# Kernel optimization log

Measured on AMD Instinct MI355X. Metric: run time of the kernel, lower is better.

Reference implementation:

```python
import jax, jax.numpy as jnp
import numpy as np

HIDDEN = 2048
NUM_HEADS = 16
NUM_KV_HEADS = 8
HEAD_DIM = 128
Q_SIZE = NUM_HEADS * HEAD_DIM          # 2048
KV_SIZE = NUM_KV_HEADS * HEAD_DIM      # 1024
ROPE_THETA = 1000000.0
RMS_EPS = 1e-6
SCALE = HEAD_DIM ** -0.5


def setup_inputs() -> dict:
    key = jax.random.key(0)
    k1, k2, k3 = jax.random.split(key, 3)
    T = 4096
    positions = jnp.arange(T, dtype=jnp.int64) if jax.config.jax_enable_x64 else jnp.arange(T, dtype=jnp.int32)
    hidden_states = jax.random.normal(k1, (T, HIDDEN), dtype=jnp.float32)
    qkv_w = jax.random.normal(k2, (Q_SIZE + 2 * KV_SIZE, HIDDEN), dtype=jnp.float32) * 0.02
    o_w = jax.random.normal(k3, (HIDDEN, Q_SIZE), dtype=jnp.float32) * 0.02
    q_norm_w = jnp.ones((HEAD_DIM,), dtype=jnp.float32)
    k_norm_w = jnp.ones((HEAD_DIM,), dtype=jnp.float32)
    return {
        "hidden_states": hidden_states,
        "qkv_w": qkv_w,
        "q_norm_w": q_norm_w,
        "k_norm_w": k_norm_w,
        "o_w": o_w,
        "positions": positions,
    }


def _rms_norm(x, w, eps=RMS_EPS):
    # per-head RMSNorm over last dim (head_dim)
    var = jnp.mean(jnp.square(x), axis=-1, keepdims=True)
    return x * jax.lax.rsqrt(var + eps) * w


def _rope(x, positions):
    # neox-style (rotate-half) RoPE. x: [T, H, D], positions: [T]
    D = x.shape[-1]
    inv_freq = 1.0 / (ROPE_THETA ** (jnp.arange(0, D, 2, dtype=jnp.float32) / D))  # [D/2]
    freqs = positions.astype(jnp.float32)[:, None] * inv_freq                      # [T, D/2]
    cos = jnp.cos(freqs)[:, None, :]  # [T, 1, D/2]
    sin = jnp.sin(freqs)[:, None, :]
    x1, x2 = x[..., : D // 2], x[..., D // 2 :]
    return jnp.concatenate([x1 * cos - x2 * sin, x2 * cos + x1 * sin], axis=-1)


def reference(hidden_states, qkv_w, q_norm_w, k_norm_w, o_w, positions):
    T = hidden_states.shape[0]
    qkv = hidden_states @ qkv_w.T                                   # [T, Q+2KV]
    q = qkv[:, :Q_SIZE].reshape(T, NUM_HEADS, HEAD_DIM)
    k = qkv[:, Q_SIZE : Q_SIZE + KV_SIZE].reshape(T, NUM_KV_HEADS, HEAD_DIM)
    v = qkv[:, Q_SIZE + KV_SIZE :].reshape(T, NUM_KV_HEADS, HEAD_DIM)

    # attention_bias=False path: per-head QK RMSNorm
    q = _rms_norm(q, q_norm_w)
    k = _rms_norm(k, k_norm_w)

    q = _rope(q, positions)
    k = _rope(k, positions)

    # GQA: expand KV heads to query heads
    rep = NUM_HEADS // NUM_KV_HEADS
    k = jnp.repeat(k, rep, axis=1)   # [T, H, D]
    v = jnp.repeat(v, rep, axis=1)

    scores = jnp.einsum("qhd,khd->hqk", q, k) * SCALE               # [H, T, T]
    causal = positions[:, None] >= positions[None, :]               # [T, T]
    scores = jnp.where(causal[None], scores, jnp.finfo(scores.dtype).min)
    probs = jax.nn.softmax(scores, axis=-1)
    attn = jnp.einsum("hqk,khd->qhd", probs, v)                     # [T, H, D]
    return attn.reshape(T, Q_SIZE) @ o_w.T                          # [T, HIDDEN]
```

## Files before the change

### kernel.cpp

```cpp
#include <hip/hip_runtime.h>
#include <hip/hip_bf16.h>
#include <math.h>


typedef __bf16 bf16;
typedef __bf16 bf16x4 __attribute__((ext_vector_type(4)));
typedef __bf16 bf16x8 __attribute__((ext_vector_type(8)));
typedef float  f32x4  __attribute__((ext_vector_type(4)));

__device__ __forceinline__ f32x4 mfma16(bf16x8 a, bf16x8 b, f32x4 c) {
  return __builtin_amdgcn_mfma_f32_16x16x32_bf16(a, b, c, 0, 0, 0);
}

__device__ __forceinline__ void mfma16x16_chain4(const bf16x4& a0, const bf16x4& a1,
                                                 const bf16x4& a2, const bf16x4& a3,
                                                 const bf16x4& b0, const bf16x4& b1,
                                                 const bf16x4& b2, const bf16x4& b3,
                                                 f32x4& c) {
  asm volatile(
      "s_nop 2\n\t"
      "v_mfma_f32_16x16x16_bf16 %0, %1, %5, %0\n\t"
      "v_mfma_f32_16x16x16_bf16 %0, %2, %6, %0\n\t"
      "v_mfma_f32_16x16x16_bf16 %0, %3, %7, %0\n\t"
      "v_mfma_f32_16x16x16_bf16 %0, %4, %8, %0"
      : "+v"(c)
      : "v"(a0), "v"(a1), "v"(a2), "v"(a3),
        "v"(b0), "v"(b1), "v"(b2), "v"(b3));
}

__device__ __forceinline__ void gload_lds16(const bf16* g, bf16* l) {
  __builtin_amdgcn_global_load_lds(
      (const __attribute__((address_space(1))) unsigned int*)g,
      (__attribute__((address_space(3))) unsigned int*)l, 16, 0, 0);
}

__device__ __forceinline__ void store_c(float* p, float v) { *p = v; }
__device__ __forceinline__ void store_c(bf16* p, float v) { *p = (bf16)v; }

__global__ __launch_bounds__(256) void cast_bf16(const float* __restrict__ s,
                                                 bf16* __restrict__ d) {
  int i = blockIdx.x * 256 + threadIdx.x;
  float4 a = reinterpret_cast<const float4*>(s)[i * 2];
  float4 b = reinterpret_cast<const float4*>(s)[i * 2 + 1];
  bf16x8 v = {(bf16)a.x, (bf16)a.y, (bf16)a.z, (bf16)a.w,
              (bf16)b.x, (bf16)b.y, (bf16)b.z, (bf16)b.w};
  reinterpret_cast<bf16x8*>(d)[i] = v;
}

__device__ __forceinline__ void gemm_step(const bf16* AsL, const bf16* BsL,
                                          int wm, int wn, int l16, int quad,
                                          f32x4 (&acc)[4][4]) {
  bf16x8 af[4], bfr[4];
#pragma unroll
  for (int i = 0; i < 4; ++i)
    af[i] = *reinterpret_cast<const bf16x8*>(&AsL[(wm + i * 16 + l16) * 32 + quad * 8]);
#pragma unroll
  for (int j = 0; j < 4; ++j)
    bfr[j] = *reinterpret_cast<const bf16x8*>(&BsL[(wn + j * 16 + l16) * 32 + quad * 8]);
#pragma unroll
  for (int i = 0; i < 4; ++i)
#pragma unroll
    for (int j = 0; j < 4; ++j)
      acc[i][j] = mfma16(af[i], bfr[j], acc[i][j]);
}

template <typename TC>
__global__ __launch_bounds__(256, 4) void gemm_bt(const bf16* __restrict__ A,
                                                  const bf16* __restrict__ B,
                                                  TC* __restrict__ C,
                                                  int M, int N, int K) {
  __shared__ __align__(16) bf16 As[2][128 * 32];
  __shared__ __align__(16) bf16 Bs[2][128 * 32];

  const int tid  = threadIdx.x;
  const int wave = tid >> 6, lane = tid & 63;
  const int quad = lane >> 4, l16 = lane & 15;
  const int wm = (wave >> 1) * 64, wn = (wave & 1) * 64;
  const int n0 = blockIdx.x * 128, m0 = blockIdx.y * 128;

  const int r0 = tid >> 2;
  const int c0 = (tid & 3) * 8;
  const size_t aBase = (size_t)(m0 + r0) * K + c0;
  const size_t bBase = (size_t)(n0 + r0) * K + c0;
  const size_t rowK64 = (size_t)64 * K;

  const f32x4 zero = {0.f, 0.f, 0.f, 0.f};
  f32x4 acc[4][4];
#pragma unroll
  for (int i = 0; i < 4; ++i)
#pragma unroll
    for (int j = 0; j < 4; ++j) acc[i][j] = zero;

  gload_lds16(&A[aBase],          &As[0][tid * 8]);
  gload_lds16(&A[aBase + rowK64], &As[0][2048 + tid * 8]);
  gload_lds16(&B[bBase],          &Bs[0][tid * 8]);
  gload_lds16(&B[bBase + rowK64], &Bs[0][2048 + tid * 8]);
  __syncthreads();

  int cur = 0;
  for (int k0 = 32; k0 < K; k0 += 32) {
    const int nb = cur ^ 1;
    gload_lds16(&A[aBase + k0],          &As[nb][tid * 8]);
    gload_lds16(&A[aBase + rowK64 + k0], &As[nb][2048 + tid * 8]);
    gload_lds16(&B[bBase + k0],          &Bs[nb][tid * 8]);
    gload_lds16(&B[bBase + rowK64 + k0], &Bs[nb][2048 + tid * 8]);

    gemm_step(As[cur], Bs[cur], wm, wn, l16, quad, acc);

    __syncthreads();
    cur = nb;
  }
  gemm_step(As[cur], Bs[cur], wm, wn, l16, quad, acc);

#pragma unroll
  for (int i = 0; i < 4; ++i)
#pragma unroll
    for (int j = 0; j < 4; ++j)
#pragma unroll
      for (int r = 0; r < 4; ++r) {
        int row = m0 + wm + i * 16 + quad * 4 + r;
        int col = n0 + wn + j * 16 + l16;
        store_c(&C[(size_t)row * N + col], acc[i][j][r]);
      }
}

__global__ __launch_bounds__(256) void norm_rope(const bf16* __restrict__ qkv,
                                                 const float* __restrict__ qw,
                                                 const float* __restrict__ kw,
                                                 const int* __restrict__ pos,
                                                 bf16* __restrict__ qn,
                                                 bf16* __restrict__ kn) {
  const int t = blockIdx.x;
  const int wv = threadIdx.x >> 6, l = threadIdx.x & 63;

  float inv = exp2f((float)l * (-19.93156856932417f / 64.0f));
  float fr = (float)pos[t] * inv;
  float sn, cs;
  sincosf(fr, &sn, &cs);
  const float qw1 = qw[l], qw2 = qw[l + 64];
  const float kw1 = kw[l], kw2 = kw[l + 64];
  const size_t rowb = (size_t)t * 4096;

#pragma unroll
  for (int i = 0; i < 6; ++i) {
    const int h = wv * 6 + i;
    const bool isq = h < 16;
    const int col = isq ? h * 128 : 2048 + (h - 16) * 128;
    float x1 = (float)qkv[rowb + col + l];
    float x2 = (float)qkv[rowb + col + l + 64];
    float ss = x1 * x1 + x2 * x2;
#pragma unroll
    for (int o = 32; o >= 1; o >>= 1) ss += __shfl_xor(ss, o);
    float rms = rsqrtf(ss * (1.0f / 128.0f) + 1e-6f);
    float w1 = isq ? qw1 : kw1, w2 = isq ? qw2 : kw2;
    float xn1 = x1 * rms * w1, xn2 = x2 * rms * w2;
    float o1 = xn1 * cs - xn2 * sn;
    float o2 = xn2 * cs + xn1 * sn;
    if (isq) {
      qn[(size_t)t * 2048 + h * 128 + l] = (bf16)o1;
      qn[(size_t)t * 2048 + h * 128 + l + 64] = (bf16)o2;
    } else {
      kn[(size_t)t * 1024 + (h - 16) * 128 + l] = (bf16)o1;
      kn[(size_t)t * 1024 + (h - 16) * 128 + l + 64] = (bf16)o2;
    }
  }
}

__global__ __launch_bounds__(256) void transpose_v(const bf16* __restrict__ qkv,
                                                   bf16* __restrict__ vt) {
  __shared__ __align__(16) bf16 tile[128 * 72];
  const int t0 = blockIdx.x * 64, kvh = blockIdx.y;
  const int tid = threadIdx.x;
#pragma unroll
  for (int it = 0; it < 2; ++it) {
    int linear = it * 4096 + tid * 16;
    int r = linear >> 7, c = linear & 127;
    union { uint4 v; bf16 e[8]; } u0, u1;
    u0.v = *reinterpret_cast<const uint4*>(
        &qkv[(size_t)(t0 + r) * 4096 + 3072 + kvh * 128 + c]);
    u1.v = *reinterpret_cast<const uint4*>(
        &qkv[(size_t)(t0 + r) * 4096 + 3072 + kvh * 128 + c + 8]);
#pragma unroll
    for (int j = 0; j < 8; ++j) tile[(c + j) * 72 + r] = u0.e[j];
#pragma unroll
    for (int j = 0; j < 8; ++j) tile[(c + 8 + j) * 72 + r] = u1.e[j];
  }
  __syncthreads();
#pragma unroll
  for (int it = 0; it < 4; ++it) {
    int linear = it * 2048 + tid * 8;
    int d = linear >> 6, c = linear & 63;
    uint4 v = *reinterpret_cast<const uint4*>(&tile[d * 72 + c]);
    *reinterpret_cast<uint4*>(&vt[(size_t)(kvh * 128 + d) * 4096 + t0 + c]) = v;
  }
}

__global__ __launch_bounds__(256, 2) void attn(const bf16* __restrict__ q,
                                               const bf16* __restrict__ k,
                                               const bf16* __restrict__ vt,
                                               bf16* __restrict__ out) {
  __shared__ __align__(16) bf16 Ks[2][64 * 128];
  __shared__ __align__(16) bf16 Vs[2][128 * 64];

  const int head = blockIdx.y, kvh = head >> 1;
  const int bx = blockIdx.x;

  const int tid = threadIdx.x;
  const int wave = tid >> 6, lane = tid & 63;
  const int quad = lane >> 4, l16 = lane & 15;
  const float cExp = 0.08838834764831845f * 1.4426950408889634f;
  const f32x4 zero = {0.f, 0.f, 0.f, 0.f};

  int kSrc[4], vSrc[4];
#pragma unroll
  for (int it = 0; it < 4; ++it) {
    int r = (wave * 4 + it) * 4 + (lane >> 4);
    kSrc[it] = r * 1024 + kvh * 128 + (((lane & 15) ^ (r & 7)) << 3);
    int d = (wave * 4 + it) * 8 + (lane >> 3);
    vSrc[it] = (kvh * 128 + d) * 4096 + (((lane & 7) ^ (lane >> 3)) << 3);
  }

  const int kswz = (l16 & 7) << 3;
  int koff[4], voff[4];
#pragma unroll
  for (int s = 0; s < 4; ++s) {
    koff[s] = (s * 32 + quad * 8) ^ kswz;
    voff[s] = (s * 16 + quad * 4) ^ kswz;
  }

#pragma unroll
  for (int it = 0; it < 4; ++it) {
    gload_lds16(&k[kSrc[it]], &Ks[0][(wave * 4 + it) * 512]);
    gload_lds16(&vt[vSrc[it]], &Vs[0][(wave * 4 + it) * 512]);
  }
  int cur = 0;

#pragma unroll
  for (int phase = 0; phase < 2; ++phase) {
    const int qt = phase == 0 ? bx : 63 - bx;
    const int q0 = qt * 64;
    const int kend = q0 + 64;
    const int qrow = q0 + wave * 16 + l16;

    bf16x8 qf[4];
#pragma unroll
    for (int s = 0; s < 4; ++s)
      qf[s] = *reinterpret_cast<const bf16x8*>(
          &q[(size_t)qrow * 2048 + head * 128 + s * 32 + quad * 8]);

    f32x4 o_acc[8];
#pragma unroll
    for (int dt = 0; dt < 8; ++dt) o_acc[dt] = zero;
    float m_i = -3.0e38f, l_i = 0.f;

    for (int k0 = 0; k0 < kend; k0 += 64) {
      __syncthreads();

      int nk0 = -1;
      if (k0 + 64 < kend)     nk0 = k0 + 64;
      else if (phase == 0)    nk0 = 0;
      if (nk0 >= 0) {
#pragma unroll
        for (int it = 0; it < 4; ++it) {
          gload_lds16(&k[kSrc[it] + nk0 * 1024],
                      &Ks[cur ^ 1][(wave * 4 + it) * 512]);
          gload_lds16(&vt[vSrc[it] + nk0],
                      &Vs[cur ^ 1][(wave * 4 + it) * 512]);
        }
      }

      const bf16* KsL = Ks[cur];
      const bf16* VsL = Vs[cur];

      f32x4 s_acc[4];
      __builtin_amdgcn_s_setprio(1);
#pragma unroll
      for (int mt = 0; mt < 4; ++mt) {
        bf16x8 kf[4];
#pragma unroll
        for (int ks = 0; ks < 4; ++ks)
          kf[ks] = *reinterpret_cast<const bf16x8*>(
              &KsL[(mt * 16 + l16) * 128 + koff[ks]]);
        f32x4 sa = zero;
#pragma unroll
        for (int ks = 0; ks < 4; ++ks) sa = mfma16(kf[ks], qf[ks], sa);
        s_acc[mt] = sa;
      }
      __builtin_amdgcn_s_setprio(0);

      if (k0 == q0) {
        int tq = wave * 16 + l16;
#pragma unroll
        for (int mt = 0; mt < 4; ++mt)
#pragma unroll
          for (int r = 0; r < 4; ++r) {
            int tk = mt * 16 + quad * 4 + r;
            if (tk > tq) s_acc[mt][r] = -3.0e38f;
          }
      }

      {
        float mx = -3.0e38f;
#pragma unroll
        for (int mt = 0; mt < 4; ++mt)
#pragma unroll
          for (int r = 0; r < 4; ++r) mx = fmaxf(mx, s_acc[mt][r]);
        mx = fmaxf(mx, __shfl_xor(mx, 16));
        mx = fmaxf(mx, __shfl_xor(mx, 32));
        if (!__all((mx - m_i) * cExp <= 8.0f)) {
          float mn = fmaxf(m_i, mx);
          float al = exp2f((m_i - mn) * cExp);
          m_i = mn;
          l_i *= al;
#pragma unroll
          for (int dt = 0; dt < 8; ++dt)
#pragma unroll
            for (int r = 0; r < 4; ++r) o_acc[dt][r] *= al;
        }
        float nmc = -m_i * cExp;
        float rs = 0.f;
#pragma unroll
        for (int mt = 0; mt < 4; ++mt)
#pragma unroll
          for (int r = 0; r < 4; ++r) {
            float pe = exp2f(fmaf(s_acc[mt][r], cExp, nmc));
            s_acc[mt][r] = pe;
            rs += pe;
          }
        rs += __shfl_xor(rs, 16);
        rs += __shfl_xor(rs, 32);
        l_i += rs;
      }

      bf16x4 pb[4];
#pragma unroll
      for (int mt = 0; mt < 4; ++mt) {
        bf16x4 t;
#pragma unroll
        for (int r = 0; r < 4; ++r) t[r] = (bf16)s_acc[mt][r];
        pb[mt] = t;
      }

      __builtin_amdgcn_s_setprio(1);
#pragma unroll
      for (int dt = 0; dt < 8; ++dt) {
        const bf16* vrow = &VsL[(dt * 16 + l16) * 64];
        bf16x4 va0 = *reinterpret_cast<const bf16x4*>(&vrow[voff[0]]);
        bf16x4 va1 = *reinterpret_cast<const bf16x4*>(&vrow[voff[1]]);
        bf16x4 va2 = *reinterpret_cast<const bf16x4*>(&vrow[voff[2]]);
        bf16x4 va3 = *reinterpret_cast<const bf16x4*>(&vrow[voff[3]]);
        mfma16x16_chain4(va0, va1, va2, va3, pb[0], pb[1], pb[2], pb[3],
                         o_acc[dt]);
      }
      __builtin_amdgcn_s_setprio(0);
      cur ^= 1;
    }

    float rl = __builtin_amdgcn_rcpf(l_i);
#pragma unroll
    for (int dt = 0; dt < 8; ++dt) {
      bf16x4 ov;
#pragma unroll
      for (int r = 0; r < 4; ++r) ov[r] = (bf16)(o_acc[dt][r] * rl);
      *reinterpret_cast<bf16x4*>(
          &out[(size_t)qrow * 2048 + head * 128 + dt * 16 + quad * 4]) = ov;
    }
  }
}

extern "C" void kernel_launch(void* const* d_in, const int* in_sizes, int n_in,
                              void* d_out, int out_size, void* d_ws, size_t ws_size,
                              hipStream_t stream) {
  const float* hidden = (const float*)d_in[0];
  const float* qkv_w  = (const float*)d_in[1];
  const float* qnw    = (const float*)d_in[2];
  const float* knw    = (const float*)d_in[3];
  const float* o_w    = (const float*)d_in[4];
  const int*   pos    = (const int*)d_in[5];

  bf16* qkv = (bf16*)d_ws;
  bf16* qn  = qkv + (size_t)4096 * 4096;
  bf16* kn  = qn  + (size_t)4096 * 2048;
  bf16* vt  = kn  + (size_t)4096 * 1024;
  bf16* ao  = vt  + (size_t)1024 * 4096;
  bf16* hb  = ao;
  bf16* wq  = kn;
  bf16* wo  = qn;
  float* out = (float*)d_out;

  cast_bf16<<<4096, 256, 0, stream>>>(hidden, hb);
  cast_bf16<<<4096, 256, 0, stream>>>(qkv_w, wq);
  gemm_bt<<<dim3(32, 32), 256, 0, stream>>>(hb, wq, qkv, 4096, 4096, 2048);
  norm_rope<<<4096, 256, 0, stream>>>(qkv, qnw, knw, pos, qn, kn);
  transpose_v<<<dim3(64, 8), 256, 0, stream>>>(qkv, vt);
  attn<<<dim3(32, 16), 256, 0, stream>>>(qn, kn, vt, ao);
  cast_bf16<<<2048, 256, 0, stream>>>(o_w, wo);
  gemm_bt<<<dim3(16, 32), 256, 0, stream>>>(ao, wo, out, 4096, 2048, 2048);
}
```

Measured before the change: 409.8 us.

## Use 256x256-tile 8-wave GEMM with XOR-swizzled LDS and staged prefetch for QKV

Adds a new GEMM kernel for the QKV projection. It uses 256x256 output tiles, 512 threads and double-buffered LDS filled by direct global-to-LDS loads. It also adds XOR-swizzled LDS columns to avoid bank conflicts, an XCD-aware block remap, and prefetches the next K tile in phases interleaved with MFMA work, with setprio around the MFMAs. The larger tile raises arithmetic intensity and cuts global traffic compared with the previous gemm_bt launch. In exchange it uses about 128KB of LDS per block, so occupancy drops to one block per CU, and it adds more barriers per K step.

```diff
diff --git a/kernel.cpp b/kernel.cpp
--- a/kernel.cpp
+++ b/kernel.cpp
@@ -47,6 +47,129 @@
   reinterpret_cast<bf16x8*>(d)[i] = v;
 }
 
+__global__ __launch_bounds__(512, 2) void gemm8ph(const bf16* __restrict__ A,
+                                                  const bf16* __restrict__ B,
+                                                  bf16* __restrict__ C,
+                                                  int M, int N, int K) {
+  __shared__ __align__(16) bf16 As[2][256 * 64];
+  __shared__ __align__(16) bf16 Bs[2][256 * 64];
+
+  const int tid  = threadIdx.x;
+  const int lane = tid & 63, wid = tid >> 6;
+  const int quad = lane >> 4, l16 = lane & 15;
+  const int wr = wid >> 2, wc = wid & 3;
+
+  const int nbx = N >> 8;
+  const int nwg = (M >> 8) * nbx;
+  const int cpx = nwg >> 3;
+  const int swz = ((int)blockIdx.x & 7) * cpx + ((int)blockIdx.x >> 3);
+  const int m0 = (swz / nbx) << 8;
+  const int n0 = (swz % nbx) << 8;
+
+  const int srow = tid >> 3;
+  const int scol = (((tid & 7) ^ (srow & 7)) << 3);
+  const bf16* aS = &A[(size_t)(m0 + srow) * K + scol];
+  const bf16* bS = &B[(size_t)(n0 + srow) * K + scol];
+  const size_t rk64 = (size_t)64 * K;
+
+  const int koff0 = ((quad)     ^ (l16 & 7)) << 3;
+  const int koff1 = ((4 + quad) ^ (l16 & 7)) << 3;
+
+  const f32x4 zero = {0.f, 0.f, 0.f, 0.f};
+  f32x4 acc[8][4];
+#pragma unroll
+  for (int i = 0; i < 8; ++i)
+#pragma unroll
+    for (int j = 0; j < 4; ++j) acc[i][j] = zero;
+
+  const int NT = K >> 6;
+
+  {
+    gload_lds16(aS,            &As[0][tid * 8]);
+    gload_lds16(aS + rk64,     &As[0][4096 + tid * 8]);
+    gload_lds16(aS + 2 * rk64, &As[0][8192 + tid * 8]);
+    gload_lds16(aS + 3 * rk64, &As[0][12288 + tid * 8]);
+    gload_lds16(bS,            &Bs[0][tid * 8]);
+    gload_lds16(bS + rk64,     &Bs[0][4096 + tid * 8]);
+    gload_lds16(bS + 2 * rk64, &Bs[0][8192 + tid * 8]);
+    gload_lds16(bS + 3 * rk64, &Bs[0][12288 + tid * 8]);
+  }
+  asm volatile("s_waitcnt vmcnt(0)" ::: "memory");
+  __builtin_amdgcn_s_barrier();
+
+  for (int t = 0; t < NT; ++t) {
+    const int c = t & 1;
+    const bf16* AsL = As[c];
+    const bf16* BsL = Bs[c];
+    const bool pre = (t + 1 < NT);
+    const size_t nk = (size_t)(t + 1) * 64;
+    bf16* An = As[c ^ 1];
+    bf16* Bn = Bs[c ^ 1];
+
+    bf16x8 bfv[4][2];
+
+#pragma unroll
+    for (int p = 0; p < 4; ++p) {
+      if (p == 0) {
+#pragma unroll
+        for (int fn = 0; fn < 4; ++fn) {
+          const bf16* bp = &BsL[(wc * 64 + fn * 16 + l16) * 64];
+          bfv[fn][0] = *reinterpret_cast<const bf16x8*>(&bp[koff0]);
+          bfv[fn][1] = *reinterpret_cast<const bf16x8*>(&bp[koff1]);
+        }
+      }
+      const bf16* ap0 = &AsL[(wr * 128 + (2 * p) * 16 + l16) * 64];
+      const bf16* ap1 = ap0 + 16 * 64;
+      bf16x8 a0k0 = *reinterpret_cast<const bf16x8*>(&ap0[koff0]);
+      bf16x8 a0k1 = *reinterpret_cast<const bf16x8*>(&ap0[koff1]);
+      bf16x8 a1k0 = *reinterpret_cast<const bf16x8*>(&ap1[koff0]);
+      bf16x8 a1k1 = *reinterpret_cast<const bf16x8*>(&ap1[koff1]);
+
+      if (p == 0 && pre) {
+        gload_lds16(aS + nk,            &An[tid * 8]);
+        gload_lds16(aS + rk64 + nk,     &An[4096 + tid * 8]);
+        gload_lds16(aS + 2 * rk64 + nk, &An[8192 + tid * 8]);
+        gload_lds16(aS + 3 * rk64 + nk, &An[12288 + tid * 8]);
+      }
+      if (p == 1 && pre) {
+        gload_lds16(bS + nk,            &Bn[tid * 8]);
+        gload_lds16(bS + rk64 + nk,     &Bn[4096 + tid * 8]);
+        gload_lds16(bS + 2 * rk64 + nk, &Bn[8192 + tid * 8]);
+        gload_lds16(bS + 3 * rk64 + nk, &Bn[12288 + tid * 8]);
+      }
+
+      __builtin_amdgcn_s_barrier();
+      __builtin_amdgcn_sched_barrier(0);
+
+      __builtin_amdgcn_s_setprio(1);
+#pragma unroll
+      for (int fn = 0; fn < 4; ++fn) {
+        acc[2 * p][fn]     = mfma16(a0k1, bfv[fn][1],
+                                    mfma16(a0k0, bfv[fn][0], acc[2 * p][fn]));
+        acc[2 * p + 1][fn] = mfma16(a1k1, bfv[fn][1],
+                                    mfma16(a1k0, bfv[fn][0], acc[2 * p + 1][fn]));
+      }
+      __builtin_amdgcn_s_setprio(0);
+
+      if (p == 3 && pre) {
+        asm volatile("s_waitcnt vmcnt(0)" ::: "memory");
+      }
+      __builtin_amdgcn_s_barrier();
+    }
+  }
+
+#pragma unroll
+  for (int fm = 0; fm < 8; ++fm)
+#pragma unroll
+    for (int fn = 0; fn < 4; ++fn)
+#pragma unroll
+      for (int r = 0; r < 4; ++r) {
+        int row = m0 + wr * 128 + fm * 16 + quad * 4 + r;
+        int col = n0 + wc * 64 + fn * 16 + l16;
+        C[(size_t)row * N + col] = (bf16)acc[fm][fn][r];
+      }
+}
+
 __device__ __forceinline__ void gemm_step(const bf16* AsL, const bf16* BsL,
                                           int wm, int wn, int l16, int quad,
                                           f32x4 (&acc)[4][4]) {
@@ -390,7 +513,7 @@
 
   cast_bf16<<<4096, 256, 0, stream>>>(hidden, hb);
   cast_bf16<<<4096, 256, 0, stream>>>(qkv_w, wq);
-  gemm_bt<<<dim3(32, 32), 256, 0, stream>>>(hb, wq, qkv, 4096, 4096, 2048);
+  gemm8ph<<<256, 512, 0, stream>>>(hb, wq, qkv, 4096, 4096, 2048);
   norm_rope<<<4096, 256, 0, stream>>>(qkv, qnw, knw, pos, qn, kn);
   transpose_v<<<dim3(64, 8), 256, 0, stream>>>(qkv, vt);
   attn<<<dim3(32, 16), 256, 0, stream>>>(qn, kn, vt, ao);
```

After: 399.1 us. 2.6% less time.

## Replace QKV projection GEMM with 256x256-tile 8-wave pipelined kernel

Applied to the files above, without the earlier changes.

Adds a new bf16 GEMM for the QKV projection that uses 256x256 output tiles, 512 threads, double-buffered LDS loaded via global_load_lds, and an XOR swizzle on the LDS layout. Each k-step is split into four phases that interleave async prefetch of the next tiles with MFMA work, plus a block-index remap for L2 locality and raised wave priority during MFMA. The goal is higher arithmetic intensity and better overlap of memory loads with matrix math than the previous 128-tile kernel. In exchange it uses large LDS (128KB) and many accumulator registers, which limits occupancy and relies on carefully hand-ordered barriers and waitcnts.

```diff
diff --git a/kernel.cpp b/kernel.cpp
--- a/kernel.cpp
+++ b/kernel.cpp
@@ -47,6 +47,133 @@
   reinterpret_cast<bf16x8*>(d)[i] = v;
 }
 
+__global__ __launch_bounds__(512, 2) void gemm8ph(const bf16* __restrict__ A,
+                                                  const bf16* __restrict__ B,
+                                                  bf16* __restrict__ C,
+                                                  int M, int N, int K) {
+  __shared__ __align__(16) bf16 As[2][256 * 64];
+  __shared__ __align__(16) bf16 Bs[2][256 * 64];
+
+  const int tid  = threadIdx.x;
+  const int lane = tid & 63, wid = tid >> 6;
+  const int quad = lane >> 4, l16 = lane & 15;
+  const int wq_r = wid >> 1, wq_c = wid & 1;
+
+  const int nbx = N >> 8;
+  const int nwg = (M >> 8) * nbx;
+  const int cpx = nwg >> 3;
+  const int swz = ((int)blockIdx.x & 7) * cpx + ((int)blockIdx.x >> 3);
+  const int m0 = (swz / nbx) << 8;
+  const int n0 = (swz % nbx) << 8;
+
+  const int srow = tid >> 3;
+  const int scol = (((tid & 7) ^ (srow & 7)) << 3);
+  const bf16* aS = &A[(size_t)(m0 + srow) * K + scol];
+  const bf16* bS = &B[(size_t)(n0 + srow) * K + scol];
+  const size_t rk64 = (size_t)64 * K;
+
+  const int koff0 = ((quad)     ^ (l16 & 7)) << 3;
+  const int koff1 = ((4 + quad) ^ (l16 & 7)) << 3;
+
+  const f32x4 zero = {0.f, 0.f, 0.f, 0.f};
+  f32x4 acc[2][2][2][4];
+#pragma unroll
+  for (int a = 0; a < 2; ++a)
+#pragma unroll
+    for (int b = 0; b < 2; ++b)
+#pragma unroll
+      for (int c = 0; c < 2; ++c)
+#pragma unroll
+        for (int d = 0; d < 4; ++d) acc[a][b][c][d] = zero;
+
+  const int NT = K >> 6;
+
+#define STAGE_A(bb, h, tt) do {                                              \
+    const size_t kk = (size_t)(tt) * 64;                                     \
+    gload_lds16(aS + (size_t)(2*(h))   * rk64 + kk, &As[bb][(2*(h))*4096   + tid*8]); \
+    gload_lds16(aS + (size_t)(2*(h)+1) * rk64 + kk, &As[bb][(2*(h)+1)*4096 + tid*8]); \
+  } while (0)
+#define STAGE_B(bb, h, tt) do {                                              \
+    const size_t kk = (size_t)(tt) * 64;                                     \
+    gload_lds16(bS + (size_t)(2*(h))   * rk64 + kk, &Bs[bb][(2*(h))*4096   + tid*8]); \
+    gload_lds16(bS + (size_t)(2*(h)+1) * rk64 + kk, &Bs[bb][(2*(h)+1)*4096 + tid*8]); \
+  } while (0)
+
+  STAGE_A(0, 0, 0); STAGE_B(0, 0, 0); STAGE_B(0, 1, 0); STAGE_A(0, 1, 0);
+  STAGE_A(1, 0, 1); STAGE_B(1, 0, 1);
+  asm volatile("s_waitcnt vmcnt(4)" ::: "memory");
+  __builtin_amdgcn_s_barrier();
+  __builtin_amdgcn_sched_barrier(0);
+
+  for (int t = 0; t < NT; ++t) {
+    const int cb = t & 1;
+    const bf16* AsL = As[cb];
+    const bf16* BsL = Bs[cb];
+    const bool s1 = (t + 1 < NT);
+    const bool s2 = (t + 2 < NT);
+
+#pragma unroll
+    for (int p = 0; p < 4; ++p) {
+      const int qm = p >> 1, qn = p & 1;
+
+      const bf16* aB = &AsL[(qm * 128 + wq_r * 32 + l16) * 64];
+      const bf16* bB = &BsL[(qn * 128 + wq_c * 64 + l16) * 64];
+      bf16x8 a0k0 = *reinterpret_cast<const bf16x8*>(&aB[koff0]);
+      bf16x8 a0k1 = *reinterpret_cast<const bf16x8*>(&aB[koff1]);
+      bf16x8 a1k0 = *reinterpret_cast<const bf16x8*>(&aB[16 * 64 + koff0]);
+      bf16x8 a1k1 = *reinterpret_cast<const bf16x8*>(&aB[16 * 64 + koff1]);
+      bf16x8 bf_[4][2];
+#pragma unroll
+      for (int fn = 0; fn < 4; ++fn) {
+        bf_[fn][0] = *reinterpret_cast<const bf16x8*>(&bB[fn * 16 * 64 + koff0]);
+        bf_[fn][1] = *reinterpret_cast<const bf16x8*>(&bB[fn * 16 * 64 + koff1]);
+      }
+
+      if (p == 0 && s1) STAGE_B(cb ^ 1, 1, t + 1);
+      if (p == 1 && s1) STAGE_A(cb ^ 1, 1, t + 1);
+      if (p == 2 && s2) STAGE_A(cb,     0, t + 2);
+      if (p == 3 && s2) STAGE_B(cb,     0, t + 2);
+
+      __builtin_amdgcn_s_barrier();
+      __builtin_amdgcn_sched_barrier(0);
+
+      __builtin_amdgcn_s_setprio(1);
+#pragma unroll
+      for (int fn = 0; fn < 4; ++fn) {
+        acc[qm][qn][0][fn] = mfma16(a0k1, bf_[fn][1],
+                                    mfma16(a0k0, bf_[fn][0], acc[qm][qn][0][fn]));
+        acc[qm][qn][1][fn] = mfma16(a1k1, bf_[fn][1],
+                                    mfma16(a1k0, bf_[fn][0], acc[qm][qn][1][fn]));
+      }
+      __builtin_amdgcn_s_setprio(0);
+
+      if (p == 3) {
+        if (s2)      asm volatile("s_waitcnt vmcnt(4)" ::: "memory");
+        else if (s1) asm volatile("s_waitcnt vmcnt(0)" ::: "memory");
+      }
+      __builtin_amdgcn_s_barrier();
+      __builtin_amdgcn_sched_barrier(0);
+    }
+  }
+#undef STAGE_A
+#undef STAGE_B
+
+#pragma unroll
+  for (int qm = 0; qm < 2; ++qm)
+#pragma unroll
+    for (int qn = 0; qn < 2; ++qn)
+#pragma unroll
+      for (int fm = 0; fm < 2; ++fm)
+#pragma unroll
+        for (int fn = 0; fn < 4; ++fn)
+#pragma unroll
+          for (int r = 0; r < 4; ++r) {
+            int row = m0 + qm * 128 + wq_r * 32 + fm * 16 + quad * 4 + r;
+            int col = n0 + qn * 128 + wq_c * 64 + fn * 16 + l16;
+            C[(size_t)row * N + col] = (bf16)acc[qm][qn][fm][fn][r];
+          }
+}
+
 __device__ __forceinline__ void gemm_step(const bf16* AsL, const bf16* BsL,
                                           int wm, int wn, int l16, int quad,
                                           f32x4 (&acc)[4][4]) {
@@ -390,7 +517,7 @@
 
   cast_bf16<<<4096, 256, 0, stream>>>(hidden, hb);
   cast_bf16<<<4096, 256, 0, stream>>>(qkv_w, wq);
-  gemm_bt<<<dim3(32, 32), 256, 0, stream>>>(hb, wq, qkv, 4096, 4096, 2048);
+  gemm8ph<<<256, 512, 0, stream>>>(hb, wq, qkv, 4096, 4096, 2048);
   norm_rope<<<4096, 256, 0, stream>>>(qkv, qnw, knw, pos, qn, kn);
   transpose_v<<<dim3(64, 8), 256, 0, stream>>>(qkv, vt);
   attn<<<dim3(32, 16), 256, 0, stream>>>(qn, kn, vt, ao);
```

Result: no change. 413.2 us (+0.8%).
